# Kernel tuning notes

Hardware: AMD Instinct MI355X
Metric: run time of the kernel (lower is better)

## Reference

```python
import jax, jax.numpy as jnp
import numpy as np

N_STEPS = 2048; WINDOW = [4, 4, 4]; INNER = 5
D_MODEL = 128; N_HEADS = 4; D_K = D_MODEL // N_HEADS
D_FFN = 512; N_LAYERS = 2; D_BOT = D_MODEL // 4; BATCH = 2
NEG = -1e9


def _mask_and_sizes():
    # faithful port of Pyraformer get_mask
    all_size = [N_STEPS]
    for w in WINDOW:
        all_size.append(all_size[-1] // w)
    S = sum(all_size)
    m = np.zeros((S, S), np.float32)
    inner = INNER // 2
    starts = [0]
    for sz in all_size:
        starts.append(starts[-1] + sz)
    for li, sz in enumerate(all_size):
        s = starts[li]
        for i in range(s, s + sz):
            m[i, max(i - inner, s):min(i + inner + 1, s + sz)] = 1
    for li in range(1, len(all_size)):
        s = starts[li]
        for i in range(s, s + all_size[li]):
            left = (s - all_size[li - 1]) + (i - s) * WINDOW[li - 1]
            right = s if i == s + all_size[li] - 1 else (s - all_size[li - 1]) + (i - s + 1) * WINDOW[li - 1]
            m[i, left:right] = 1
            m[left:right, i] = 1
    return (1 - m).astype(bool), all_size  # True = masked out


def _refer_points(all_size):
    # faithful port of Pyraformer refer_points -> [n_steps, n_levels]
    idx = np.zeros((N_STEPS, len(all_size)), np.int32)
    for i in range(N_STEPS):
        idx[i, 0] = i
        former = i
        for j in range(1, len(all_size)):
            start = int(sum(all_size[:j]))
            inner_idx = former - (start - all_size[j - 1])
            former = start + min(inner_idx // WINDOW[j - 1], all_size[j] - 1)
            idx[i, j] = former
    return idx


def _ln(x, g, b, eps):
    mu = jnp.mean(x, -1, keepdims=True)
    var = jnp.mean((x - mu) ** 2, -1, keepdims=True)
    return (x - mu) * jax.lax.rsqrt(var + eps) * g + b


def setup_inputs() -> dict:
    key = jax.random.key(0)
    ks = jax.random.split(key, 12)
    mask_np, all_size = _mask_and_sizes()
    idx_np = _refer_points(all_size)
    s = 0.02
    rn = lambda k, shape: jax.random.normal(k, shape, jnp.float32) * s
    L, W = N_LAYERS, len(WINDOW)
    return {
        'x': jax.random.normal(ks[0], (BATCH, N_STEPS, D_MODEL), jnp.float32),
        'w_down': rn(ks[1], (D_MODEL, D_BOT)), 'b_down': jnp.zeros((D_BOT,)),
        'conv_w': rn(ks[2], (W, D_BOT, D_BOT, WINDOW[0])), 'conv_b': jnp.zeros((W, D_BOT)),
        'bn_g': jnp.ones((W, D_BOT)), 'bn_b': jnp.zeros((W, D_BOT)),
        'bn_m': jnp.zeros((W, D_BOT)), 'bn_v': jnp.ones((W, D_BOT)),
        'w_up': rn(ks[3], (D_BOT, D_MODEL)), 'b_up': jnp.zeros((D_MODEL,)),
        'ln0_g': jnp.ones((D_MODEL,)), 'ln0_b': jnp.zeros((D_MODEL,)),
        'wq': rn(ks[4], (L, D_MODEL, N_HEADS * D_K)), 'wk': rn(ks[5], (L, D_MODEL, N_HEADS * D_K)),
        'wv': rn(ks[6], (L, D_MODEL, N_HEADS * D_K)), 'wo': rn(ks[7], (L, N_HEADS * D_K, D_MODEL)),
        'ln1_g': jnp.ones((L, D_MODEL)), 'ln1_b': jnp.zeros((L, D_MODEL)),
        'ffn_w1': rn(ks[8], (L, D_MODEL, D_FFN)), 'ffn_b1': jnp.zeros((L, D_FFN)),
        'ffn_w2': rn(ks[9], (L, D_FFN, D_MODEL)), 'ffn_b2': jnp.zeros((L, D_MODEL)),
        'ln2_g': jnp.ones((L, D_MODEL)), 'ln2_b': jnp.zeros((L, D_MODEL)),
        'mask': jnp.asarray(mask_np), 'indexes': jnp.asarray(idx_np),
    }


def _fwd(mask, indexes, x, w_down, b_down, conv_w, conv_b, bn_g, bn_b, bn_m, bn_v,
         w_up, b_up, ln0_g, ln0_b, wq, wk, wv, wo, ln1_g, ln1_b,
         ffn_w1, ffn_b1, ffn_w2, ffn_b2, ln2_g, ln2_b):
    B = x.shape[0]
    # Bottleneck_Construct: down-proj, strided convs per scale, up-proj, concat, LN
    t = (x @ w_down + b_down).transpose(0, 2, 1)  # [B, d_bot, N]
    outs = []
    for i in range(len(WINDOW)):
        t = jax.lax.conv_general_dilated(t, conv_w[i], (WINDOW[i],), 'VALID',
                                         dimension_numbers=('NCH', 'OIH', 'NCH'))
        t = t + conv_b[i][None, :, None]
        t = (t - bn_m[i][None, :, None]) * jax.lax.rsqrt(bn_v[i][None, :, None] + 1e-5) \
            * bn_g[i][None, :, None] + bn_b[i][None, :, None]  # BatchNorm1d (eval)
        t = jax.nn.elu(t)
        outs.append(t)
    pooled = jnp.concatenate(outs, axis=2).transpose(0, 2, 1)  # [B, 672, d_bot]
    h = jnp.concatenate([x, pooled @ w_up + b_up], axis=1)  # [B, S=2720, d_model]
    h = _ln(h, ln0_g, ln0_b, 1e-5)
    S = h.shape[1]
    mask4 = mask[None, None]  # [1,1,S,S], True = masked
    inv_temp = 1.0 / np.float32(np.sqrt(D_K))
    for l in range(N_LAYERS):
        q = (h @ wq[l]).reshape(B, S, N_HEADS, D_K).transpose(0, 2, 1, 3)
        k = (h @ wk[l]).reshape(B, S, N_HEADS, D_K).transpose(0, 2, 1, 3)
        v = (h @ wv[l]).reshape(B, S, N_HEADS, D_K).transpose(0, 2, 1, 3)
        attn = jnp.einsum('bhqd,bhkd->bhqk', q * inv_temp, k)
        attn = jnp.where(mask4, NEG, attn)
        attn = jax.nn.softmax(attn, axis=-1)
        o = jnp.einsum('bhqk,bhkd->bhqd', attn, v).transpose(0, 2, 1, 3).reshape(B, S, N_HEADS * D_K)
        h = _ln(h + o @ wo[l], ln1_g[l], ln1_b[l], 1e-6)
        f = jax.nn.relu(h @ ffn_w1[l] + ffn_b1[l]) @ ffn_w2[l] + ffn_b2[l]
        h = _ln(h + f, ln2_g[l], ln2_b[l], 1e-6)
    # multi-scale gather reassembly (refer_points)
    idx_flat = indexes.reshape(-1)  # [n_steps * n_levels]
    all_enc = h[:, idx_flat, :]  # [B, n_steps*levels, d_model]
    return all_enc.reshape(B, N_STEPS, -1)  # [B, n_steps, levels*d_model]


def reference(x, mask, indexes, w_down, b_down, conv_w, conv_b, bn_g, bn_b, bn_m, bn_v,
              w_up, b_up, ln0_g, ln0_b, wq, wk, wv, wo, ln1_g, ln1_b,
              ffn_w1, ffn_b1, ffn_w2, ffn_b2, ln2_g, ln2_b):
    return _fwd(mask, indexes, x, w_down, b_down, conv_w, conv_b, bn_g, bn_b, bn_m, bn_v,
                w_up, b_up, ln0_g, ln0_b, wq, wk, wv, wo, ln1_g, ln1_b,
                ffn_w1, ffn_b1, ffn_w2, ffn_b2, ln2_g, ln2_b)
```

## Files before the change

kernel.cpp:

```cpp
#include <hip/hip_runtime.h>
#include <hip/hip_bf16.h>

#define S_TOT 2720

typedef short bf16x8 __attribute__((ext_vector_type(8)));
typedef float f32x4 __attribute__((ext_vector_type(4)));

__global__ void cvt_all_kernel(const float* __restrict__ w1, const float* __restrict__ w2,
                               const float* __restrict__ wq, const float* __restrict__ wk,
                               const float* __restrict__ wv, const float* __restrict__ wo,
                               __hip_bfloat16* __restrict__ out) {
    int id = blockIdx.x * 256 + threadIdx.x;
    if (id < 131072) {
        int l = id >> 16, r = id & 65535;
        int j = r >> 7, k = r & 127;
        out[id] = __float2bfloat16(w1[l * 65536 + k * 512 + j]);
    } else if (id < 262144) {
        int t = id - 131072;
        int l = t >> 16, r = t & 65535;
        int d = r >> 9, j = r & 511;
        out[id] = __float2bfloat16(w2[l * 65536 + j * 128 + d]);
    } else if (id < 360448) {
        int t = id - 262144;
        int l = t / 49152, r = t % 49152;
        int m = r >> 14, rr = r & 16383;
        int j = rr >> 7, k = rr & 127;
        const float* W = (m == 0) ? wq : (m == 1) ? wk : wv;
        out[id] = __float2bfloat16(W[l * 16384 + k * 128 + j]);
    } else {
        int t = id - 360448;
        int l = t >> 14, r = t & 16383;
        int j = r >> 7, k = r & 127;
        out[id] = __float2bfloat16(wo[l * 16384 + k * 128 + j]);
    }
}

__global__ void down_kernel(const float* __restrict__ x, const float* __restrict__ w,
                            const float* __restrict__ b, float* __restrict__ t0) {
    int id = blockIdx.x * 256 + threadIdx.x;
    int c = id & 31;
    int r = id >> 5;
    const float* xr = x + (size_t)r * 128;
    float a0 = b[c], a1 = 0.f, a2 = 0.f, a3 = 0.f;
#pragma unroll
    for (int k = 0; k < 128; k += 4) {
        a0 += xr[k]     * w[(k)     * 32 + c];
        a1 += xr[k + 1] * w[(k + 1) * 32 + c];
        a2 += xr[k + 2] * w[(k + 2) * 32 + c];
        a3 += xr[k + 3] * w[(k + 3) * 32 + c];
    }
    t0[id] = (a0 + a1) + (a2 + a3);
}

__global__ void conv_kernel(const float* __restrict__ in, float* __restrict__ pooled,
                            const float* __restrict__ cw, const float* __restrict__ cb,
                            const float* __restrict__ bg, const float* __restrict__ bb,
                            const float* __restrict__ bm, const float* __restrict__ bv,
                            int level, int in_bstride, int in_off, int Lout, int out_off,
                            int total) {
    int id = blockIdx.x * 256 + threadIdx.x;
    if (id >= total) return;
    int co = id & 31;
    int lo = (id >> 5) % Lout;
    int b  = id / (32 * Lout);
    const float* ib = in + (size_t)(b * in_bstride + in_off + lo * 4) * 32;
    const float* w  = cw + (size_t)(level * 32 + co) * 32 * 4;
    float acc0 = 0.f, acc1 = 0.f, acc2 = 0.f, acc3 = 0.f;
#pragma unroll
    for (int ci = 0; ci < 32; ++ci) {
        acc0 += ib[0 * 32 + ci] * w[ci * 4 + 0];
        acc1 += ib[1 * 32 + ci] * w[ci * 4 + 1];
        acc2 += ib[2 * 32 + ci] * w[ci * 4 + 2];
        acc3 += ib[3 * 32 + ci] * w[ci * 4 + 3];
    }
    float acc = ((acc0 + acc1) + (acc2 + acc3)) + cb[level * 32 + co];
    acc = (acc - bm[level * 32 + co]) * rsqrtf(bv[level * 32 + co] + 1e-5f)
          * bg[level * 32 + co] + bb[level * 32 + co];
    acc = acc > 0.f ? acc : expm1f(acc);
    pooled[(size_t)(b * 672 + out_off + lo) * 32 + co] = acc;
}

__global__ void build_ln_kernel(const float* __restrict__ x, const float* __restrict__ pooled,
                                const float* __restrict__ w_up, const float* __restrict__ b_up,
                                const float* __restrict__ g, const float* __restrict__ bta,
                                float* __restrict__ h) {
    int wave = threadIdx.x >> 6;
    int lane = threadIdx.x & 63;
    int row = blockIdx.x * 4 + wave;
    int b = row / S_TOT, s = row % S_TOT;
    float v0, v1;
    if (s < 2048) {
        const float* xr = x + (size_t)(b * 2048 + s) * 128;
        v0 = xr[lane]; v1 = xr[lane + 64];
    } else {
        int p = s - 2048;
        const float* pr = pooled + (size_t)(b * 672 + p) * 32;
        float a0 = b_up[lane], a1 = b_up[lane + 64];
        float a2 = 0.f, a3 = 0.f;
#pragma unroll
        for (int k = 0; k < 32; k += 2) {
            float p0 = pr[k], p1 = pr[k + 1];
            a0 += p0 * w_up[k * 128 + lane];
            a1 += p0 * w_up[k * 128 + lane + 64];
            a2 += p1 * w_up[(k + 1) * 128 + lane];
            a3 += p1 * w_up[(k + 1) * 128 + lane + 64];
        }
        v0 = a0 + a2; v1 = a1 + a3;
    }
    float sum = v0 + v1;
#pragma unroll
    for (int off = 32; off; off >>= 1) sum += __shfl_xor(sum, off);
    float mu = sum * (1.f / 128.f);
    float d0 = v0 - mu, d1 = v1 - mu;
    float vs = d0 * d0 + d1 * d1;
#pragma unroll
    for (int off = 32; off; off >>= 1) vs += __shfl_xor(vs, off);
    float inv = rsqrtf(vs * (1.f / 128.f) + 1e-5f);
    h[(size_t)row * 128 + lane]      = d0 * inv * g[lane]      + bta[lane];
    h[(size_t)row * 128 + lane + 64] = d1 * inv * g[lane + 64] + bta[lane + 64];
}

__global__ __launch_bounds__(256) void qkv_mfma_kernel(const float* __restrict__ H,
                                                       const __hip_bfloat16* __restrict__ wqkvt,
                                                       float* __restrict__ q,
                                                       float* __restrict__ k,
                                                       float* __restrict__ v) {
    __shared__ __hip_bfloat16 hsb[16][136];
    int tid = threadIdx.x;
    int r0 = blockIdx.x * 16;
    {
        int row = tid >> 4, c0 = (tid & 15) * 8;
        const float* src = &H[(size_t)(r0 + row) * 128 + c0];
        float4 x0 = *(const float4*)src;
        float4 x1 = *(const float4*)(src + 4);
        __hip_bfloat16* d = &hsb[row][c0];
        d[0] = __float2bfloat16(x0.x); d[1] = __float2bfloat16(x0.y);
        d[2] = __float2bfloat16(x0.z); d[3] = __float2bfloat16(x0.w);
        d[4] = __float2bfloat16(x1.x); d[5] = __float2bfloat16(x1.y);
        d[6] = __float2bfloat16(x1.z); d[7] = __float2bfloat16(x1.w);
    }
    __syncthreads();
    int lane = tid & 63, wv = tid >> 6;
    int l15 = lane & 15, grp = lane >> 4;
    bf16x8 afr[4];
#pragma unroll
    for (int ks = 0; ks < 4; ++ks)
        afr[ks] = *(const bf16x8*)&hsb[l15][ks * 32 + grp * 8];
    float* O[3] = {q, k, v};
#pragma unroll
    for (int t = 0; t < 6; ++t) {
        int gt = wv * 6 + t;
        int mat = gt >> 3, jj = gt & 7;
        int j0 = jj * 16;
        f32x4 acc = {0.f, 0.f, 0.f, 0.f};
        const __hip_bfloat16* wb = &wqkvt[(size_t)(mat * 128 + j0 + l15) * 128 + grp * 8];
#pragma unroll
        for (int ks = 0; ks < 4; ++ks) {
            bf16x8 bfr = *(const bf16x8*)&wb[ks * 32];
            acc = __builtin_amdgcn_mfma_f32_16x16x32_bf16(afr[ks], bfr, acc, 0, 0, 0);
        }
        float* Om = O[mat];
#pragma unroll
        for (int i = 0; i < 4; ++i)
            Om[(size_t)(r0 + grp * 4 + i) * 128 + j0 + l15] = acc[i];
    }
}

__global__ void attn_kernel(const float* __restrict__ Q, const float* __restrict__ K,
                            const float* __restrict__ V, float* __restrict__ O) {
    int id = blockIdx.x * 256 + threadIdx.x;
    int d0 = (id & 3) * 8;
    int gid = id >> 2;
    int i  = gid % S_TOT;
    int hh = (gid / S_TOT) & 3;
    int b  = gid / (S_TOT * 4);
    int li, s;
    if (i < 2048)      { li = 0; s = 0;    }
    else if (i < 2560) { li = 1; s = 2048; }
    else if (i < 2688) { li = 2; s = 2560; }
    else               { li = 3; s = 2688; }
    int sz = (li == 0) ? 2048 : (li == 1) ? 512 : (li == 2) ? 128 : 32;
    int pstart = (li == 0) ? 2048 : (li == 1) ? 2560 : 2688;
    int cstart = (li == 1) ? 0 : (li == 2) ? 2048 : 2560;

    const float* qp = Q + ((size_t)(b * S_TOT + i) * 128) + hh * 32 + d0;
    float4 qa = *(const float4*)qp;
    float4 qb = *(const float4*)(qp + 4);
    const float invt = 0.17677669529663687f;

    float sc[10];
    int   nj[10];
    bool  vl[10];
#pragma unroll
    for (int slot = 0; slot < 10; ++slot) {
        int j; bool valid;
        if (slot < 5)       { j = i - 2 + slot;                         valid = (j >= s) && (j < s + sz); }
        else if (slot == 5) { j = pstart + ((i - s) >> 2);              valid = (li < 3); }
        else                { j = cstart + ((i - s) << 2) + (slot - 6); valid = (li > 0); }
        nj[slot] = j; vl[slot] = valid;
        float dot = 0.f;
        if (valid) {
            const float* kp = K + ((size_t)(b * S_TOT + j) * 128) + hh * 32 + d0;
            float4 ka = *(const float4*)kp;
            float4 kb = *(const float4*)(kp + 4);
            dot = qa.x * ka.x + qa.y * ka.y + qa.z * ka.z + qa.w * ka.w
                + qb.x * kb.x + qb.y * kb.y + qb.z * kb.z + qb.w * kb.w;
        }
        dot += __shfl_xor(dot, 1);
        dot += __shfl_xor(dot, 2);
        sc[slot] = valid ? dot * invt : -1e30f;
    }
    float mx = sc[0];
#pragma unroll
    for (int slot = 1; slot < 10; ++slot) mx = fmaxf(mx, sc[slot]);
    float ssum = 0.f;
#pragma unroll
    for (int slot = 0; slot < 10; ++slot) { sc[slot] = __expf(sc[slot] - mx); ssum += sc[slot]; }
    float rinv = 1.f / ssum;
    float4 oa = {0.f, 0.f, 0.f, 0.f}, ob = {0.f, 0.f, 0.f, 0.f};
#pragma unroll
    for (int slot = 0; slot < 10; ++slot) {
        if (vl[slot]) {
            float p = sc[slot] * rinv;
            const float* vp = V + ((size_t)(b * S_TOT + nj[slot]) * 128) + hh * 32 + d0;
            float4 va = *(const float4*)vp;
            float4 vb = *(const float4*)(vp + 4);
            oa.x += p * va.x; oa.y += p * va.y; oa.z += p * va.z; oa.w += p * va.w;
            ob.x += p * vb.x; ob.y += p * vb.y; ob.z += p * vb.z; ob.w += p * vb.w;
        }
    }
    float* op = O + ((size_t)(b * S_TOT + i) * 128) + hh * 32 + d0;
    *(float4*)op = oa;
    *(float4*)(op + 4) = ob;
}

__global__ __launch_bounds__(256) void o_ffn_mfma_kernel(const float* __restrict__ Ob,
                                                         const __hip_bfloat16* __restrict__ wot,
                                                         const float* __restrict__ g1,
                                                         const float* __restrict__ b1ta,
                                                         const __hip_bfloat16* __restrict__ w1t,
                                                         const float* __restrict__ b1,
                                                         const __hip_bfloat16* __restrict__ w2t,
                                                         const float* __restrict__ b2,
                                                         const float* __restrict__ g2,
                                                         const float* __restrict__ b2ta,
                                                         float* __restrict__ h) {
    __shared__ __hip_bfloat16 osb[16][136];
    __shared__ __hip_bfloat16 pb[16][520];
    __shared__ float partf[16][128];
    __shared__ float h1s[16][128];
    int tid = threadIdx.x;
    int r0 = blockIdx.x * 16;
    {
        int row = tid >> 4, c0 = (tid & 15) * 8;
        const float* src = &Ob[(size_t)(r0 + row) * 128 + c0];
        float4 x0 = *(const float4*)src;
        float4 x1 = *(const float4*)(src + 4);
        __hip_bfloat16* d = &osb[row][c0];
        d[0] = __float2bfloat16(x0.x); d[1] = __float2bfloat16(x0.y);
        d[2] = __float2bfloat16(x0.z); d[3] = __float2bfloat16(x0.w);
        d[4] = __float2bfloat16(x1.x); d[5] = __float2bfloat16(x1.y);
        d[6] = __float2bfloat16(x1.z); d[7] = __float2bfloat16(x1.w);
    }
    __syncthreads();
    int lane = tid & 63, wv = tid >> 6;
    int l15 = lane & 15, grp = lane >> 4;
    {
        bf16x8 afr[4];
#pragma unroll
        for (int ks = 0; ks < 4; ++ks)
            afr[ks] = *(const bf16x8*)&osb[l15][ks * 32 + grp * 8];
#pragma unroll
        for (int t = 0; t < 2; ++t) {
            int j0 = (wv * 2 + t) * 16;
            f32x4 acc = {0.f, 0.f, 0.f, 0.f};
            const __hip_bfloat16* wb = &wot[(size_t)(j0 + l15) * 128 + grp * 8];
#pragma unroll
            for (int ks = 0; ks < 4; ++ks) {
                bf16x8 bfr = *(const bf16x8*)&wb[ks * 32];
                acc = __builtin_amdgcn_mfma_f32_16x16x32_bf16(afr[ks], bfr, acc, 0, 0, 0);
            }
#pragma unroll
            for (int i = 0; i < 4; ++i)
                partf[grp * 4 + i][j0 + l15] = acc[i];
        }
    }
    __syncthreads();
    {
        int r = tid >> 4, d0 = (tid & 15) * 8;
        size_t row = (size_t)(r0 + r) * 128;
        float vv[8];
        float sum = 0.f;
#pragma unroll
        for (int i = 0; i < 8; ++i) {
            int d = d0 + i;
            vv[i] = partf[r][d] + h[row + d];
            sum += vv[i];
        }
#pragma unroll
        for (int off = 8; off; off >>= 1) sum += __shfl_xor(sum, off);
        float mu = sum * (1.f / 128.f);
        float vs = 0.f;
#pragma unroll
        for (int i = 0; i < 8; ++i) { vv[i] -= mu; vs += vv[i] * vv[i]; }
#pragma unroll
        for (int off = 8; off; off >>= 1) vs += __shfl_xor(vs, off);
        float inv = rsqrtf(vs * (1.f / 128.f) + 1e-6f);
        __hip_bfloat16* db = &osb[r][d0];
#pragma unroll
        for (int i = 0; i < 8; ++i) {
            float hv = vv[i] * inv * g1[d0 + i] + b1ta[d0 + i];
            h1s[r][d0 + i] = hv;
            db[i] = __float2bfloat16(hv);
        }
    }
    __syncthreads();
    {
        bf16x8 afr[4];
#pragma unroll
        for (int ks = 0; ks < 4; ++ks)
            afr[ks] = *(const bf16x8*)&osb[l15][ks * 32 + grp * 8];
#pragma unroll
        for (int t = 0; t < 8; ++t) {
            int j0 = (wv * 8 + t) * 16;
            f32x4 acc = {0.f, 0.f, 0.f, 0.f};
            const __hip_bfloat16* wb = &w1t[(size_t)(j0 + l15) * 128 + grp * 8];
#pragma unroll
            for (int ks = 0; ks < 4; ++ks) {
                bf16x8 bfr = *(const bf16x8*)&wb[ks * 32];
                acc = __builtin_amdgcn_mfma_f32_16x16x32_bf16(afr[ks], bfr, acc, 0, 0, 0);
            }
            float bv = b1[j0 + l15];
#pragma unroll
            for (int i = 0; i < 4; ++i)
                pb[grp * 4 + i][j0 + l15] = __float2bfloat16(fmaxf(acc[i] + bv, 0.f));
        }
    }
    __syncthreads();
    {
        f32x4 acc2a = {0.f, 0.f, 0.f, 0.f};
        f32x4 acc2b = {0.f, 0.f, 0.f, 0.f};
        const __hip_bfloat16* wb0 = &w2t[(size_t)(wv * 32 + l15) * 512 + grp * 8];
        const __hip_bfloat16* wb1 = &w2t[(size_t)(wv * 32 + 16 + l15) * 512 + grp * 8];
#pragma unroll
        for (int ks = 0; ks < 16; ++ks) {
            bf16x8 afr2 = *(const bf16x8*)&pb[l15][ks * 32 + grp * 8];
            bf16x8 b0 = *(const bf16x8*)&wb0[ks * 32];
            bf16x8 b1f = *(const bf16x8*)&wb1[ks * 32];
            acc2a = __builtin_amdgcn_mfma_f32_16x16x32_bf16(afr2, b0, acc2a, 0, 0, 0);
            acc2b = __builtin_amdgcn_mfma_f32_16x16x32_bf16(afr2, b1f, acc2b, 0, 0, 0);
        }
#pragma unroll
        for (int i = 0; i < 4; ++i) {
            partf[grp * 4 + i][wv * 32 + l15]      = acc2a[i];
            partf[grp * 4 + i][wv * 32 + 16 + l15] = acc2b[i];
        }
    }
    __syncthreads();
    {
        int r = tid >> 4, d0 = (tid & 15) * 8;
        size_t row = (size_t)(r0 + r) * 128;
        float vv[8];
        float sum = 0.f;
#pragma unroll
        for (int i = 0; i < 8; ++i) {
            int d = d0 + i;
            vv[i] = partf[r][d] + b2[d] + h1s[r][d];
            sum += vv[i];
        }
#pragma unroll
        for (int off = 8; off; off >>= 1) sum += __shfl_xor(sum, off);
        float mu = sum * (1.f / 128.f);
        float vs = 0.f;
#pragma unroll
        for (int i = 0; i < 8; ++i) { vv[i] -= mu; vs += vv[i] * vv[i]; }
#pragma unroll
        for (int off = 8; off; off >>= 1) vs += __shfl_xor(vs, off);
        float inv = rsqrtf(vs * (1.f / 128.f) + 1e-6f);
#pragma unroll
        for (int i = 0; i < 8; ++i) vv[i] = vv[i] * inv * g2[d0 + i] + b2ta[d0 + i];
        *(float4*)&h[row + d0]     = make_float4(vv[0], vv[1], vv[2], vv[3]);
        *(float4*)&h[row + d0 + 4] = make_float4(vv[4], vv[5], vv[6], vv[7]);
    }
}

__global__ void gather_kernel(const float* __restrict__ H, const int* __restrict__ idx,
                              float* __restrict__ out) {
    int id = blockIdx.x * 256 + threadIdx.x;
    int d4 = id & 31;
    int j = (id >> 5) & 3;
    int t = (id >> 7) & 2047;
    int b = id >> 18;
    int src = idx[t * 4 + j];
    ((float4*)out)[id] = *(const float4*)&H[((size_t)(b * S_TOT + src) * 128) + d4 * 4];
}

extern "C" void kernel_launch(void* const* d_in, const int* in_sizes, int n_in,
                              void* d_out, int out_size, void* d_ws, size_t ws_size,
                              hipStream_t stream) {
    (void)in_sizes; (void)n_in; (void)out_size; (void)ws_size;
    const float* x       = (const float*)d_in[0];
    const float* w_down  = (const float*)d_in[1];
    const float* b_down  = (const float*)d_in[2];
    const float* conv_w  = (const float*)d_in[3];
    const float* conv_b  = (const float*)d_in[4];
    const float* bn_g    = (const float*)d_in[5];
    const float* bn_b    = (const float*)d_in[6];
    const float* bn_m    = (const float*)d_in[7];
    const float* bn_v    = (const float*)d_in[8];
    const float* w_up    = (const float*)d_in[9];
    const float* b_up    = (const float*)d_in[10];
    const float* ln0_g   = (const float*)d_in[11];
    const float* ln0_b   = (const float*)d_in[12];
    const float* wq      = (const float*)d_in[13];
    const float* wk      = (const float*)d_in[14];
    const float* wv      = (const float*)d_in[15];
    const float* wo      = (const float*)d_in[16];
    const float* ln1_g   = (const float*)d_in[17];
    const float* ln1_b   = (const float*)d_in[18];
    const float* ffn_w1  = (const float*)d_in[19];
    const float* ffn_b1  = (const float*)d_in[20];
    const float* ffn_w2  = (const float*)d_in[21];
    const float* ffn_b2  = (const float*)d_in[22];
    const float* ln2_g   = (const float*)d_in[23];
    const float* ln2_b   = (const float*)d_in[24];
    const int* indexes   = (const int*)d_in[26];

    float* ws = (float*)d_ws;
    float* t0     = ws;
    float* pooled = ws + 131072;
    float* h      = ws + 174080;
    float* q      = ws + 870400;
    float* k      = ws + 1566720;
    float* v      = ws + 2263040;
    float* o      = ws + 2959360;
    __hip_bfloat16* wb_all = (__hip_bfloat16*)(ws + 3655680);
    __hip_bfloat16* w1t   = wb_all;
    __hip_bfloat16* w2t   = wb_all + 131072;
    __hip_bfloat16* wqkvt = wb_all + 262144;
    __hip_bfloat16* wot   = wb_all + 360448;

    cvt_all_kernel<<<1536, 256, 0, stream>>>(ffn_w1, ffn_w2, wq, wk, wv, wo, wb_all);

    down_kernel<<<512, 256, 0, stream>>>(x, w_down, b_down, t0);
    conv_kernel<<<128, 256, 0, stream>>>(t0, pooled, conv_w, conv_b, bn_g, bn_b, bn_m, bn_v,
                                         0, 2048, 0, 512, 0, 32768);
    conv_kernel<<<32, 256, 0, stream>>>(pooled, pooled, conv_w, conv_b, bn_g, bn_b, bn_m, bn_v,
                                        1, 672, 0, 128, 512, 8192);
    conv_kernel<<<8, 256, 0, stream>>>(pooled, pooled, conv_w, conv_b, bn_g, bn_b, bn_m, bn_v,
                                       2, 672, 512, 32, 640, 2048);
    build_ln_kernel<<<1360, 256, 0, stream>>>(x, pooled, w_up, b_up, ln0_g, ln0_b, h);

    for (int l = 0; l < 2; ++l) {
        qkv_mfma_kernel<<<340, 256, 0, stream>>>(h, wqkvt + l * 49152, q, k, v);
        attn_kernel<<<340, 256, 0, stream>>>(q, k, v, o);
        o_ffn_mfma_kernel<<<340, 256, 0, stream>>>(o, wot + l * 16384,
                                                   ln1_g + l * 128, ln1_b + l * 128,
                                                   w1t + l * 65536, ffn_b1 + l * 512,
                                                   w2t + l * 65536, ffn_b2 + l * 128,
                                                   ln2_g + l * 128, ln2_b + l * 128, h);
    }
    gather_kernel<<<2048, 256, 0, stream>>>(h, indexes, (float*)d_out);
}
```

Before: 127.1 us.

## Fuse sparse attention into the output-projection and FFN kernel

Moves the pyramidal sparse-attention computation into the start of the o-projection/FFN kernel. Each 16-row block computes its attention outputs directly into shared memory as bf16 instead of writing an fp32 O buffer to global memory and reading it back. This drops one kernel launch per layer and one round trip of the attention output through global memory. The cost is a heavier fused kernel that may keep more registers live, which could lower occupancy.

```diff
diff --git a/kernel.cpp b/kernel.cpp
--- a/kernel.cpp
+++ b/kernel.cpp
@@ -166,75 +166,9 @@
     }
 }
 
-__global__ void attn_kernel(const float* __restrict__ Q, const float* __restrict__ K,
-                            const float* __restrict__ V, float* __restrict__ O) {
-    int id = blockIdx.x * 256 + threadIdx.x;
-    int d0 = (id & 3) * 8;
-    int gid = id >> 2;
-    int i  = gid % S_TOT;
-    int hh = (gid / S_TOT) & 3;
-    int b  = gid / (S_TOT * 4);
-    int li, s;
-    if (i < 2048)      { li = 0; s = 0;    }
-    else if (i < 2560) { li = 1; s = 2048; }
-    else if (i < 2688) { li = 2; s = 2560; }
-    else               { li = 3; s = 2688; }
-    int sz = (li == 0) ? 2048 : (li == 1) ? 512 : (li == 2) ? 128 : 32;
-    int pstart = (li == 0) ? 2048 : (li == 1) ? 2560 : 2688;
-    int cstart = (li == 1) ? 0 : (li == 2) ? 2048 : 2560;
-
-    const float* qp = Q + ((size_t)(b * S_TOT + i) * 128) + hh * 32 + d0;
-    float4 qa = *(const float4*)qp;
-    float4 qb = *(const float4*)(qp + 4);
-    const float invt = 0.17677669529663687f;
-
-    float sc[10];
-    int   nj[10];
-    bool  vl[10];
-#pragma unroll
-    for (int slot = 0; slot < 10; ++slot) {
-        int j; bool valid;
-        if (slot < 5)       { j = i - 2 + slot;                         valid = (j >= s) && (j < s + sz); }
-        else if (slot == 5) { j = pstart + ((i - s) >> 2);              valid = (li < 3); }
-        else                { j = cstart + ((i - s) << 2) + (slot - 6); valid = (li > 0); }
-        nj[slot] = j; vl[slot] = valid;
-        float dot = 0.f;
-        if (valid) {
-            const float* kp = K + ((size_t)(b * S_TOT + j) * 128) + hh * 32 + d0;
-            float4 ka = *(const float4*)kp;
-            float4 kb = *(const float4*)(kp + 4);
-            dot = qa.x * ka.x + qa.y * ka.y + qa.z * ka.z + qa.w * ka.w
-                + qb.x * kb.x + qb.y * kb.y + qb.z * kb.z + qb.w * kb.w;
-        }
-        dot += __shfl_xor(dot, 1);
-        dot += __shfl_xor(dot, 2);
-        sc[slot] = valid ? dot * invt : -1e30f;
-    }
-    float mx = sc[0];
-#pragma unroll
-    for (int slot = 1; slot < 10; ++slot) mx = fmaxf(mx, sc[slot]);
-    float ssum = 0.f;
-#pragma unroll
-    for (int slot = 0; slot < 10; ++slot) { sc[slot] = __expf(sc[slot] - mx); ssum += sc[slot]; }
-    float rinv = 1.f / ssum;
-    float4 oa = {0.f, 0.f, 0.f, 0.f}, ob = {0.f, 0.f, 0.f, 0.f};
-#pragma unroll
-    for (int slot = 0; slot < 10; ++slot) {
-        if (vl[slot]) {
-            float p = sc[slot] * rinv;
-            const float* vp = V + ((size_t)(b * S_TOT + nj[slot]) * 128) + hh * 32 + d0;
-            float4 va = *(const float4*)vp;
-            float4 vb = *(const float4*)(vp + 4);
-            oa.x += p * va.x; oa.y += p * va.y; oa.z += p * va.z; oa.w += p * va.w;
-            ob.x += p * vb.x; ob.y += p * vb.y; ob.z += p * vb.z; ob.w += p * vb.w;
-        }
-    }
-    float* op = O + ((size_t)(b * S_TOT + i) * 128) + hh * 32 + d0;
-    *(float4*)op = oa;
-    *(float4*)(op + 4) = ob;
-}
-
-__global__ __launch_bounds__(256) void o_ffn_mfma_kernel(const float* __restrict__ Ob,
+__global__ __launch_bounds__(256) void attn_o_ffn_kernel(const float* __restrict__ Q,
+                                                         const float* __restrict__ K,
+                                                         const float* __restrict__ V,
                                                          const __hip_bfloat16* __restrict__ wot,
                                                          const float* __restrict__ g1,
                                                          const float* __restrict__ b1ta,
@@ -252,15 +186,72 @@
     int tid = threadIdx.x;
     int r0 = blockIdx.x * 16;
     {
-        int row = tid >> 4, c0 = (tid & 15) * 8;
-        const float* src = &Ob[(size_t)(r0 + row) * 128 + c0];
-        float4 x0 = *(const float4*)src;
-        float4 x1 = *(const float4*)(src + 4);
-        __hip_bfloat16* d = &osb[row][c0];
-        d[0] = __float2bfloat16(x0.x); d[1] = __float2bfloat16(x0.y);
-        d[2] = __float2bfloat16(x0.z); d[3] = __float2bfloat16(x0.w);
-        d[4] = __float2bfloat16(x1.x); d[5] = __float2bfloat16(x1.y);
-        d[6] = __float2bfloat16(x1.z); d[7] = __float2bfloat16(x1.w);
+        int rl = tid >> 4;
+        int hh = (tid >> 2) & 3;
+        int qd = tid & 3;
+        int d0 = qd * 8;
+        int row = r0 + rl;
+        int b = row / S_TOT, i = row % S_TOT;
+        int li, s;
+        if (i < 2048)      { li = 0; s = 0;    }
+        else if (i < 2560) { li = 1; s = 2048; }
+        else if (i < 2688) { li = 2; s = 2560; }
+        else               { li = 3; s = 2688; }
+        int sz = (li == 0) ? 2048 : (li == 1) ? 512 : (li == 2) ? 128 : 32;
+        int pstart = (li == 0) ? 2048 : (li == 1) ? 2560 : 2688;
+        int cstart = (li == 1) ? 0 : (li == 2) ? 2048 : 2560;
+
+        const float* qp = Q + ((size_t)row * 128) + hh * 32 + d0;
+        float4 qa = *(const float4*)qp;
+        float4 qb = *(const float4*)(qp + 4);
+        const float invt = 0.17677669529663687f;
+
+        float sc[10];
+        int   nj[10];
+        bool  vl[10];
+#pragma unroll
+        for (int slot = 0; slot < 10; ++slot) {
+            int j; bool valid;
+            if (slot < 5)       { j = i - 2 + slot;                         valid = (j >= s) && (j < s + sz); }
+            else if (slot == 5) { j = pstart + ((i - s) >> 2);              valid = (li < 3); }
+            else                { j = cstart + ((i - s) << 2) + (slot - 6); valid = (li > 0); }
+            nj[slot] = j; vl[slot] = valid;
+            float dot = 0.f;
+            if (valid) {
+                const float* kp = K + ((size_t)(b * S_TOT + j) * 128) + hh * 32 + d0;
+                float4 ka = *(const float4*)kp;
+                float4 kb = *(const float4*)(kp + 4);
+                dot = qa.x * ka.x + qa.y * ka.y + qa.z * ka.z + qa.w * ka.w
+                    + qb.x * kb.x + qb.y * kb.y + qb.z * kb.z + qb.w * kb.w;
+            }
+            dot += __shfl_xor(dot, 1);
+            dot += __shfl_xor(dot, 2);
+            sc[slot] = valid ? dot * invt : -1e30f;
+        }
+        float mx = sc[0];
+#pragma unroll
+        for (int slot = 1; slot < 10; ++slot) mx = fmaxf(mx, sc[slot]);
+        float ssum = 0.f;
+#pragma unroll
+        for (int slot = 0; slot < 10; ++slot) { sc[slot] = __expf(sc[slot] - mx); ssum += sc[slot]; }
+        float rinv = 1.f / ssum;
+        float4 oa = {0.f, 0.f, 0.f, 0.f}, ob = {0.f, 0.f, 0.f, 0.f};
+#pragma unroll
+        for (int slot = 0; slot < 10; ++slot) {
+            if (vl[slot]) {
+                float p = sc[slot] * rinv;
+                const float* vp = V + ((size_t)(b * S_TOT + nj[slot]) * 128) + hh * 32 + d0;
+                float4 va = *(const float4*)vp;
+                float4 vb = *(const float4*)(vp + 4);
+                oa.x += p * va.x; oa.y += p * va.y; oa.z += p * va.z; oa.w += p * va.w;
+                ob.x += p * vb.x; ob.y += p * vb.y; ob.z += p * vb.z; ob.w += p * vb.w;
+            }
+        }
+        __hip_bfloat16* dst = &osb[rl][hh * 32 + d0];
+        dst[0] = __float2bfloat16(oa.x); dst[1] = __float2bfloat16(oa.y);
+        dst[2] = __float2bfloat16(oa.z); dst[3] = __float2bfloat16(oa.w);
+        dst[4] = __float2bfloat16(ob.x); dst[5] = __float2bfloat16(ob.y);
+        dst[6] = __float2bfloat16(ob.z); dst[7] = __float2bfloat16(ob.w);
     }
     __syncthreads();
     int lane = tid & 63, wv = tid >> 6;
@@ -433,8 +424,7 @@
     float* q      = ws + 870400;
     float* k      = ws + 1566720;
     float* v      = ws + 2263040;
-    float* o      = ws + 2959360;
-    __hip_bfloat16* wb_all = (__hip_bfloat16*)(ws + 3655680);
+    __hip_bfloat16* wb_all = (__hip_bfloat16*)(ws + 2959360);
     __hip_bfloat16* w1t   = wb_all;
     __hip_bfloat16* w2t   = wb_all + 131072;
     __hip_bfloat16* wqkvt = wb_all + 262144;
@@ -453,8 +443,7 @@
 
     for (int l = 0; l < 2; ++l) {
         qkv_mfma_kernel<<<340, 256, 0, stream>>>(h, wqkvt + l * 49152, q, k, v);
-        attn_kernel<<<340, 256, 0, stream>>>(q, k, v, o);
-        o_ffn_mfma_kernel<<<340, 256, 0, stream>>>(o, wot + l * 16384,
+        attn_o_ffn_kernel<<<340, 256, 0, stream>>>(q, k, v, wot + l * 16384,
                                                    ln1_g + l * 128, ln1_b + l * 128,
                                                    w1t + l * 65536, ffn_b1 + l * 512,
                                                    w2t + l * 65536, ffn_b2 + l * 128,
```

Result: faster. 114.9 us (-9.6%).
